# Kernel optimization log

Measured on AMD Instinct MI355X. Metric: run time of the kernel, lower is better.

The kernel has to match this reference:

```python
import jax, jax.numpy as jnp
import numpy as np

L, B, S, D, H, FF, V, P = 6, 8, 1024, 768, 12, 3072, 50257, 1024
DH = D // H
EPS = 1e-5


def setup_inputs() -> dict:
    key = jax.random.key(0)
    ks = jax.random.split(key, 12)
    std = 0.02
    return {
        "x_ids": jax.random.randint(ks[0], (B, S), 0, V),
        "calibrated_mask": jax.random.normal(ks[1], (B, S, S), jnp.float32),
        "wte": jax.random.normal(ks[2], (V, D), jnp.float32) * std,
        "wpe": jax.random.normal(ks[3], (P, D), jnp.float32) * std,
        "ln1_g": jnp.ones((L, D), jnp.float32),
        "ln1_b": jnp.zeros((L, D), jnp.float32),
        "qkv_w": jax.random.normal(ks[4], (L, D, 3 * D), jnp.float32) * std,
        "qkv_b": jnp.zeros((L, 3 * D), jnp.float32),
        "ao_w": jax.random.normal(ks[5], (L, D, D), jnp.float32) * std,
        "ao_b": jnp.zeros((L, D), jnp.float32),
        "ln2_g": jnp.ones((L, D), jnp.float32),
        "ln2_b": jnp.zeros((L, D), jnp.float32),
        "fc_w": jax.random.normal(ks[6], (L, D, FF), jnp.float32) * std,
        "fc_b": jnp.zeros((L, FF), jnp.float32),
        "op_w": jax.random.normal(ks[7], (L, FF, D), jnp.float32) * std,
        "op_b": jnp.zeros((L, D), jnp.float32),
        "lnf_g": jnp.ones((D,), jnp.float32),
        "lnf_b": jnp.zeros((D,), jnp.float32),
    }


def _ln(x, g, b):
    m = jnp.mean(x, axis=-1, keepdims=True)
    v = jnp.var(x, axis=-1, keepdims=True)
    return (x - m) * jax.lax.rsqrt(v + EPS) * g + b


def _gelu_new(x):
    c = np.sqrt(2.0 / np.pi).astype(np.float32)
    return 0.5 * x * (1.0 + jnp.tanh(c * (x + 0.044715 * x * x * x)))


def _gpt2_forward(x_ids, calibrated_mask, wte, wpe, ln1_g, ln1_b, qkv_w, qkv_b,
                  ao_w, ao_b, ln2_g, ln2_b, fc_w, fc_b, op_w, op_b, lnf_g, lnf_b):
    s = x_ids.shape[1]
    h = wte[x_ids] + wpe[:s][None, :, :]  # [B,S,D]
    causal = jnp.tril(jnp.ones((s, s), bool))
    neg = jnp.finfo(h.dtype).min
    # additive mask, broadcast over heads (unsqueeze(1).repeat over n_head)
    add_mask = calibrated_mask[:, None, :, :]  # [B,1,S,S]

    def block(hid, p):
        l1g, l1b, qw, qb, aw, ab, l2g, l2b, fw, fb, ow, ob = p
        x = _ln(hid, l1g, l1b)
        qkv = x @ qw + qb  # [B,S,3D]
        q, k, v = jnp.split(qkv, 3, axis=-1)
        q = q.reshape(q.shape[0], s, H, DH).transpose(0, 2, 1, 3)
        k = k.reshape(k.shape[0], s, H, DH).transpose(0, 2, 1, 3)
        v = v.reshape(v.shape[0], s, H, DH).transpose(0, 2, 1, 3)
        scores = jnp.einsum('bhqd,bhkd->bhqk', q, k) / jnp.sqrt(jnp.asarray(DH, q.dtype))
        scores = jnp.where(causal[None, None], scores, neg)
        scores = scores + add_mask
        w = jax.nn.softmax(scores, axis=-1)
        a = jnp.einsum('bhqk,bhkd->bhqd', w, v)
        a = a.transpose(0, 2, 1, 3).reshape(a.shape[0], s, D)
        hid = hid + a @ aw + ab
        x2 = _ln(hid, l2g, l2b)
        hid = hid + _gelu_new(x2 @ fw + fb) @ ow + ob
        return hid, None

    params = (ln1_g, ln1_b, qkv_w, qkv_b, ao_w, ao_b, ln2_g, ln2_b, fc_w, fc_b, op_w, op_b)
    h, _ = jax.lax.scan(block, h, params)
    return _ln(h, lnf_g, lnf_b)


def reference(x_ids, calibrated_mask, wte, wpe, ln1_g, ln1_b, qkv_w, qkv_b,
              ao_w, ao_b, ln2_g, ln2_b, fc_w, fc_b, op_w, op_b, lnf_g, lnf_b):
    return _gpt2_forward(x_ids, calibrated_mask, wte, wpe, ln1_g, ln1_b, qkv_w, qkv_b,
                         ao_w, ao_b, ln2_g, ln2_b, fc_w, fc_b, op_w, op_b, lnf_g, lnf_b)
```

## Files before the change

### kernel.cpp

```cpp
#include <hip/hip_runtime.h>
#include <hip/hip_bf16.h>

typedef __bf16 bf16_t;
typedef __bf16 bf16x8 __attribute__((ext_vector_type(8)));
typedef __bf16 bf16x4 __attribute__((ext_vector_type(4)));
typedef float  f32x4  __attribute__((ext_vector_type(4)));

#define DEV __device__ __forceinline__

DEV void gload_lds16(const void* g, void* l) {
  __builtin_amdgcn_global_load_lds(
      (__attribute__((address_space(1))) void*)(void*)g,
      (__attribute__((address_space(3))) void*)l, 16, 0, 0);
}

__global__ __launch_bounds__(256)
void transpose_cast(const float* __restrict__ in, bf16_t* __restrict__ out,
                    int K, int N) {
  __shared__ float tile[32][33];
  const long z = blockIdx.z;
  const float* inz = in + z * (long)K * N;
  bf16_t* outz = out + z * (long)N * K;
  const int k0 = blockIdx.x * 32;
  const int n0 = blockIdx.y * 32;
  const int tx = threadIdx.x;
  const int ty = threadIdx.y;
#pragma unroll
  for (int i = 0; i < 32; i += 8)
    tile[ty + i][tx] = inz[(long)(k0 + ty + i) * N + n0 + tx];
  __syncthreads();
#pragma unroll
  for (int i = 0; i < 32; i += 8)
    outz[(long)(n0 + ty + i) * K + k0 + tx] = (bf16_t)tile[tx][ty + i];
}

__global__ __launch_bounds__(256)
void embed_kernel(const int* __restrict__ ids, const float* __restrict__ wte,
                  const float* __restrict__ wpe, bf16_t* __restrict__ h) {
  const int t = blockIdx.x * 256 + threadIdx.x;
  const int row = t / 96;
  const int c8  = (t % 96) * 8;
  const int s   = row & 1023;
  const float* wr = wte + (long)ids[row] * 768 + c8;
  const float* pr = wpe + (long)s * 768 + c8;
  bf16x8 o;
#pragma unroll
  for (int j = 0; j < 8; ++j) o[j] = (bf16_t)(wr[j] + pr[j]);
  *(bf16x8*)&h[(long)row * 768 + c8] = o;
}

template <bool BF16OUT>
__global__ __launch_bounds__(256)
void ln_kernel(const bf16_t* __restrict__ x, const float* __restrict__ g,
               const float* __restrict__ b, bf16_t* __restrict__ ob,
               float* __restrict__ of) {
  const int lane = threadIdx.x & 63;
  const long row = blockIdx.x * 4 + (threadIdx.x >> 6);
  const bf16_t* xr = x + row * 768;
  const bf16x8 v8 = *(const bf16x8*)&xr[lane * 8];
  const bf16x4 v4 = *(const bf16x4*)&xr[512 + lane * 4];
  float vv[12];
#pragma unroll
  for (int j = 0; j < 8; ++j) vv[j] = (float)v8[j];
#pragma unroll
  for (int j = 0; j < 4; ++j) vv[8 + j] = (float)v4[j];
  float s = 0.f, sq = 0.f;
#pragma unroll
  for (int j = 0; j < 12; ++j) { s += vv[j]; sq += vv[j] * vv[j]; }
#pragma unroll
  for (int o = 32; o; o >>= 1) { s += __shfl_xor(s, o); sq += __shfl_xor(sq, o); }
  const float mean = s * (1.f / 768.f);
  const float rs = rsqrtf(sq * (1.f / 768.f) - mean * mean + 1e-5f);
  if (BF16OUT) {
    bf16x8 o8; bf16x4 o4;
#pragma unroll
    for (int j = 0; j < 8; ++j) {
      const int col = lane * 8 + j;
      o8[j] = (bf16_t)((vv[j] - mean) * rs * g[col] + b[col]);
    }
#pragma unroll
    for (int j = 0; j < 4; ++j) {
      const int col = 512 + lane * 4 + j;
      o4[j] = (bf16_t)((vv[8 + j] - mean) * rs * g[col] + b[col]);
    }
    *(bf16x8*)&ob[row * 768 + lane * 8] = o8;
    *(bf16x4*)&ob[row * 768 + 512 + lane * 4] = o4;
  } else {
#pragma unroll
    for (int j = 0; j < 8; ++j) {
      const int col = lane * 8 + j;
      of[row * 768 + col] = (vv[j] - mean) * rs * g[col] + b[col];
    }
#pragma unroll
    for (int j = 0; j < 4; ++j) {
      const int col = 512 + lane * 4 + j;
      of[row * 768 + col] = (vv[8 + j] - mean) * rs * g[col] + b[col];
    }
  }
}

template <int EPI, int BN>
__global__ __launch_bounds__(256, 4)
void gemm_bt(const bf16_t* __restrict__ A, const bf16_t* __restrict__ Bt,
             const float* __restrict__ bias, bf16_t* __restrict__ Cb,
             int M, int N, int K) {
  constexpr int NI = BN / 32;
  __shared__ bf16_t As[128 * 64];
  __shared__ bf16_t Bs[BN * 64];
  const int tid  = threadIdx.x;
  const int lane = tid & 63, w = tid >> 6;
  const int col = lane & 15, s16 = lane >> 4;
  const int nbn = N / BN;
  const int cpx = gridDim.x >> 3;
  const int bid = (blockIdx.x & 7) * cpx + (blockIdx.x >> 3);
  const int bm = bid / nbn, bn = bid % nbn;
  const int wr = w >> 1, wc = w & 1;

  f32x4 acc[4][NI];
#pragma unroll
  for (int i = 0; i < 4; ++i)
#pragma unroll
    for (int j = 0; j < NI; ++j) acc[i][j] = f32x4{0.f, 0.f, 0.f, 0.f};

  const long arow0 = (long)bm * 128;
  const long brow0 = (long)bn * BN;

  const int nt = K >> 6;
  for (int t = 0; t < nt; ++t) {
    const int k0 = t << 6;
#pragma unroll
    for (int i = 0; i < 4; ++i) {
      const int c = i * 256 + tid;
      const int row = c >> 3, slot = c & 7;
      gload_lds16(A + (arow0 + row) * (long)K + k0 + ((slot ^ (row & 7)) << 3),
                  (char*)As + c * 16);
    }
#pragma unroll
    for (int i = 0; i < BN / 32; ++i) {
      const int c = i * 256 + tid;
      const int row = c >> 3, slot = c & 7;
      gload_lds16(Bt + (brow0 + row) * (long)K + k0 + ((slot ^ (row & 7)) << 3),
                  (char*)Bs + c * 16);
    }
    __syncthreads();

    bf16x8 af[2][4], bfr[2][NI];
#pragma unroll
    for (int mi = 0; mi < 4; ++mi) {
      const int row = wr * 64 + mi * 16 + col;
#pragma unroll
      for (int ks = 0; ks < 2; ++ks) {
        const int slot = ks * 4 + s16;
        af[ks][mi] = *(const bf16x8*)((char*)As + row * 128 +
                                      ((slot ^ (row & 7)) << 4));
      }
    }
#pragma unroll
    for (int ni = 0; ni < NI; ++ni) {
      const int row = wc * (BN / 2) + ni * 16 + col;
#pragma unroll
      for (int ks = 0; ks < 2; ++ks) {
        const int slot = ks * 4 + s16;
        bfr[ks][ni] = *(const bf16x8*)((char*)Bs + row * 128 +
                                       ((slot ^ (row & 7)) << 4));
      }
    }
#pragma unroll
    for (int ks = 0; ks < 2; ++ks)
#pragma unroll
      for (int mi = 0; mi < 4; ++mi)
#pragma unroll
        for (int ni = 0; ni < NI; ++ni)
          acc[mi][ni] = __builtin_amdgcn_mfma_f32_16x16x32_bf16(
              af[ks][mi], bfr[ks][ni], acc[mi][ni], 0, 0, 0);

    __syncthreads();
  }

  const int colb = bn * BN + wc * (BN / 2) + col;
  const int rowb = bm * 128 + wr * 64 + (s16 << 2);
#pragma unroll
  for (int ni = 0; ni < NI; ++ni) {
    const int ccol = colb + ni * 16;
    const float bv = bias[ccol];
#pragma unroll
    for (int mi = 0; mi < 4; ++mi) {
      const int row = rowb + mi * 16;
#pragma unroll
      for (int r = 0; r < 4; ++r) {
        const float v = acc[mi][ni][r] + bv;
        const long idx = (long)(row + r) * N + ccol;
        if (EPI == 1) {
          Cb[idx] = (bf16_t)((float)Cb[idx] + v);
        } else if (EPI == 2) {
          Cb[idx] = (bf16_t)v;
        } else {
          const float z = 0.7978845608028654f * (v + 0.044715f * v * v * v);
          Cb[idx] = (bf16_t)(v / (1.f + __expf(-2.f * z)));
        }
      }
    }
  }
}

template <int EPI>
__global__ __launch_bounds__(512, 4)
void gemm_bw(const bf16_t* __restrict__ A, const bf16_t* __restrict__ Bt,
             const float* __restrict__ bias, bf16_t* __restrict__ Cb,
             int M, int N, int K) {
  __shared__ bf16_t As[256 * 64];
  __shared__ bf16_t Bs[128 * 64];
  const int tid = threadIdx.x;
  const int lane = tid & 63, w = tid >> 6;
  const int col = lane & 15, s16 = lane >> 4;
  const int wm = w >> 1, wn = w & 1;
  const int nbn = N >> 7;
  const int cpx = gridDim.x >> 3;
  const int bid = (blockIdx.x & 7) * cpx + (blockIdx.x >> 3);
  const int bm = bid / nbn, bn = bid % nbn;
  const long arow0 = (long)bm * 256, brow0 = (long)bn * 128;

  f32x4 acc[4][4];
#pragma unroll
  for (int i = 0; i < 4; ++i)
#pragma unroll
    for (int j = 0; j < 4; ++j) acc[i][j] = f32x4{0.f, 0.f, 0.f, 0.f};

  const int nt = K >> 6;
  for (int t = 0; t < nt; ++t) {
    const int k0 = t << 6;
#pragma unroll
    for (int i = 0; i < 4; ++i) {
      const int c = i * 512 + tid;
      const int row = c >> 3, slot = c & 7;
      gload_lds16(A + (arow0 + row) * (long)K + k0 + ((slot ^ (row & 7)) << 3),
                  (char*)As + c * 16);
    }
#pragma unroll
    for (int i = 0; i < 2; ++i) {
      const int c = i * 512 + tid;
      const int row = c >> 3, slot = c & 7;
      gload_lds16(Bt + (brow0 + row) * (long)K + k0 + ((slot ^ (row & 7)) << 3),
                  (char*)Bs + c * 16);
    }
    __syncthreads();

    bf16x8 af[2][4], bfr[2][4];
#pragma unroll
    for (int mi = 0; mi < 4; ++mi) {
      const int row = wm * 64 + mi * 16 + col;
#pragma unroll
      for (int ks = 0; ks < 2; ++ks) {
        const int slot = ks * 4 + s16;
        af[ks][mi] = *(const bf16x8*)((char*)As + row * 128 +
                                      ((slot ^ (row & 7)) << 4));
      }
    }
#pragma unroll
    for (int ni = 0; ni < 4; ++ni) {
      const int row = wn * 64 + ni * 16 + col;
#pragma unroll
      for (int ks = 0; ks < 2; ++ks) {
        const int slot = ks * 4 + s16;
        bfr[ks][ni] = *(const bf16x8*)((char*)Bs + row * 128 +
                                       ((slot ^ (row & 7)) << 4));
      }
    }
#pragma unroll
    for (int ks = 0; ks < 2; ++ks)
#pragma unroll
      for (int mi = 0; mi < 4; ++mi)
#pragma unroll
        for (int ni = 0; ni < 4; ++ni)
          acc[mi][ni] = __builtin_amdgcn_mfma_f32_16x16x32_bf16(
              af[ks][mi], bfr[ks][ni], acc[mi][ni], 0, 0, 0);

    __syncthreads();
  }

  const int rowb = bm * 256 + wm * 64 + (s16 << 2);
  const int colb = bn * 128 + wn * 64 + col;
#pragma unroll
  for (int ni = 0; ni < 4; ++ni) {
    const int ccol = colb + ni * 16;
    const float bv = bias[ccol];
#pragma unroll
    for (int mi = 0; mi < 4; ++mi) {
      const int row = rowb + mi * 16;
#pragma unroll
      for (int r = 0; r < 4; ++r) {
        const float v = acc[mi][ni][r] + bv;
        if (EPI == 2) Cb[(long)(row + r) * N + ccol] = (bf16_t)v;
        else {
          const float z = 0.7978845608028654f * (v + 0.044715f * v * v * v);
          Cb[(long)(row + r) * N + ccol] = (bf16_t)(v / (1.f + __expf(-2.f * z)));
        }
      }
    }
  }
}

__global__ __launch_bounds__(256, 3)
void attn_kernel(const bf16_t* __restrict__ qkv, const float* __restrict__ mask,
                 bf16_t* __restrict__ out) {
  __shared__ bf16_t Kl[2][64 * 64];
  __shared__ bf16_t Vt[2][64 * 64];
  __shared__ bf16_t Pl[4][16 * 64];
  const int tid = threadIdx.x, lane = tid & 63, w = tid >> 6;
  const int col = lane & 15, s16 = lane >> 4, l7 = lane & 7;
  const int qp = blockIdx.x & 7;
  const int bh = blockIdx.x >> 3;
  const int b = bh / 12, h = bh % 12;
  const int sw0 = (s16 ^ l7) << 4;
  const int sw1 = ((s16 + 4) ^ l7) << 4;
  char* const plw = (char*)&Pl[w][0];
  const long qkvb = (long)b * 1024 * 2304;

  auto stageK = [&](int buf, int k0) {
#pragma unroll
    for (int i = 0; i < 2; ++i) {
      const int c = i * 256 + tid;
      const int krow = c >> 3, slot = c & 7;
      gload_lds16(qkv + qkvb + (long)(k0 + krow) * 2304 + 768 + h * 64 +
                      ((slot ^ (krow & 7)) << 3),
                  (char*)&Kl[buf][0] + i * 4096 + w * 1024);
    }
  };
  auto loadV = [&](int k0, bf16x8& t0, bf16x8& t1) {
    const bf16_t* vbase = qkv + qkvb + 1536 + h * 64;
#pragma unroll
    for (int i = 0; i < 2; ++i) {
      const int c = i * 256 + tid;
      const int d = c & 63, koct = c >> 6;
      const bf16_t* vsrc = vbase + (long)(k0 + koct * 8) * 2304 + d;
      bf16x8 tv;
#pragma unroll
      for (int j = 0; j < 8; ++j) tv[j] = vsrc[(long)j * 2304];
      if (i == 0) t0 = tv; else t1 = tv;
    }
  };
  auto storeV = [&](int buf, const bf16x8& t0, const bf16x8& t1) {
#pragma unroll
    for (int i = 0; i < 2; ++i) {
      const int c = i * 256 + tid;
      const int d = c & 63, koct = c >> 6;
      *(bf16x8*)((char*)&Vt[buf][0] + d * 128 + ((koct ^ (d & 7)) << 4)) =
          (i == 0) ? t0 : t1;
    }
  };

#pragma unroll 1
  for (int pass = 0; pass < 2; ++pass) {
    const int qt = pass ? (15 - qp) : qp;
    const int qrow0 = qt * 64 + w * 16;
    const long rowQ = (long)(b * 1024 + qrow0 + col) * 2304 + h * 64;
    const bf16x8 aq0 = *(const bf16x8*)&qkv[rowQ + s16 * 8];
    const bf16x8 aq1 = *(const bf16x8*)&qkv[rowQ + 32 + s16 * 8];
    const int qb = qrow0 + s16 * 4;
    const float* mrow = mask + ((long)b * 1024 + qb) * 1024;

    auto loadM = [&](int k0, float (&m)[4][4]) {
#pragma unroll
      for (int g = 0; g < 4; ++g)
#pragma unroll
        for (int r = 0; r < 4; ++r)
          m[g][r] = mrow[(long)r * 1024 + k0 + g * 16 + col];
    };

    float m_run[4], l_run[4];
    f32x4 o_acc[4];
#pragma unroll
    for (int r = 0; r < 4; ++r) { m_run[r] = -INFINITY; l_run[r] = 0.f; }
#pragma unroll
    for (int go = 0; go < 4; ++go) o_acc[go] = f32x4{0.f, 0.f, 0.f, 0.f};

    bf16x8 tv0, tv1;
    stageK(0, 0);
    loadV(0, tv0, tv1);
    storeV(0, tv0, tv1);
    float msk[4][4];
    loadM(0, msk);
    __syncthreads();

#pragma unroll 1
    for (int kt = 0; kt <= qt; ++kt) {
      const int cur = kt & 1;
      const bool more = kt < qt;
      const int k0 = kt * 64;
      float mnx[4][4];
      if (more) {
        stageK(cur ^ 1, k0 + 64);
        loadV(k0 + 64, tv0, tv1);
        loadM(k0 + 64, mnx);
      }

      f32x4 sf[4];
      __builtin_amdgcn_s_setprio(1);
#pragma unroll
      for (int g = 0; g < 4; ++g) {
        const int rbyte = (g * 16 + col) * 128;
        bf16x8 bk0 = *(const bf16x8*)((char*)&Kl[cur][0] + rbyte + sw0);
        bf16x8 bk1 = *(const bf16x8*)((char*)&Kl[cur][0] + rbyte + sw1);
        f32x4 z = f32x4{0.f, 0.f, 0.f, 0.f};
        z = __builtin_amdgcn_mfma_f32_16x16x32_bf16(aq0, bk0, z, 0, 0, 0);
        z = __builtin_amdgcn_mfma_f32_16x16x32_bf16(aq1, bk1, z, 0, 0, 0);
        sf[g] = z;
      }
      __builtin_amdgcn_s_setprio(0);

      const bool diag = (kt == qt);
      float sv[4][4];
#pragma unroll
      for (int g = 0; g < 4; ++g)
#pragma unroll
        for (int r = 0; r < 4; ++r) {
          float s = sf[g][r] * 0.125f + msk[g][r];
          if (diag && (k0 + g * 16 + col) > (qb + r)) s = -INFINITY;
          sv[g][r] = s;
        }
#pragma unroll
      for (int r = 0; r < 4; ++r) {
        float mx = fmaxf(fmaxf(sv[0][r], sv[1][r]), fmaxf(sv[2][r], sv[3][r]));
#pragma unroll
        for (int o = 8; o; o >>= 1) mx = fmaxf(mx, __shfl_xor(mx, o));
        const float m_new = fmaxf(m_run[r], mx);
        const float f = __expf(m_run[r] - m_new);
        m_run[r] = m_new;
        float sum = 0.f;
#pragma unroll
        for (int g = 0; g < 4; ++g) {
          const float p = __expf(sv[g][r] - m_new);
          sv[g][r] = p;
          sum += p;
        }
#pragma unroll
        for (int o = 8; o; o >>= 1) sum += __shfl_xor(sum, o);
        l_run[r] = l_run[r] * f + sum;
#pragma unroll
        for (int go = 0; go < 4; ++go) o_acc[go][r] *= f;
      }

#pragma unroll
      for (int g = 0; g < 4; ++g) {
        const int ks = 2 * g + (col >> 3);
#pragma unroll
        for (int r = 0; r < 4; ++r) {
          const int qr = s16 * 4 + r;
          *(bf16_t*)(plw + qr * 128 + ((ks ^ (qr & 7)) << 4) + l7 * 2) = (bf16_t)sv[g][r];
        }
      }
      const bf16x8 pa0 = *(const bf16x8*)(plw + col * 128 + sw0);
      const bf16x8 pa1 = *(const bf16x8*)(plw + col * 128 + sw1);
      __builtin_amdgcn_s_setprio(1);
#pragma unroll
      for (int go = 0; go < 4; ++go) {
        const int dbyte = (go * 16 + col) * 128;
        bf16x8 bv0 = *(const bf16x8*)((char*)&Vt[cur][0] + dbyte + sw0);
        bf16x8 bv1 = *(const bf16x8*)((char*)&Vt[cur][0] + dbyte + sw1);
        o_acc[go] = __builtin_amdgcn_mfma_f32_16x16x32_bf16(pa0, bv0, o_acc[go], 0, 0, 0);
        o_acc[go] = __builtin_amdgcn_mfma_f32_16x16x32_bf16(pa1, bv1, o_acc[go], 0, 0, 0);
      }
      __builtin_amdgcn_s_setprio(0);

      if (more) {
        storeV(cur ^ 1, tv0, tv1);
#pragma unroll
        for (int g = 0; g < 4; ++g)
#pragma unroll
          for (int r = 0; r < 4; ++r) msk[g][r] = mnx[g][r];
      }
      __syncthreads();
    }

    float inv[4];
#pragma unroll
    for (int r = 0; r < 4; ++r) inv[r] = 1.f / l_run[r];
#pragma unroll
    for (int go = 0; go < 4; ++go)
#pragma unroll
      for (int r = 0; r < 4; ++r)
        out[(long)(b * 1024 + qb + r) * 768 + h * 64 + go * 16 + col] =
            (bf16_t)(o_acc[go][r] * inv[r]);
  }
}

extern "C" void kernel_launch(void* const* d_in, const int* in_sizes, int n_in,
                              void* d_out, int out_size, void* d_ws, size_t ws_size,
                              hipStream_t stream) {
  const int*   x_ids = (const int*)d_in[0];
  const float* mask  = (const float*)d_in[1];
  const float* wte   = (const float*)d_in[2];
  const float* wpe   = (const float*)d_in[3];
  const float* ln1_g = (const float*)d_in[4];
  const float* ln1_b = (const float*)d_in[5];
  const float* qkv_w = (const float*)d_in[6];
  const float* qkv_b = (const float*)d_in[7];
  const float* ao_w  = (const float*)d_in[8];
  const float* ao_b  = (const float*)d_in[9];
  const float* ln2_g = (const float*)d_in[10];
  const float* ln2_b = (const float*)d_in[11];
  const float* fc_w  = (const float*)d_in[12];
  const float* fc_b  = (const float*)d_in[13];
  const float* op_w  = (const float*)d_in[14];
  const float* op_b  = (const float*)d_in[15];
  const float* lnf_g = (const float*)d_in[16];
  const float* lnf_b = (const float*)d_in[17];

  char* ws = (char*)d_ws;
  size_t off = 0;
  auto alloc = [&](size_t bytes) {
    char* p = ws + off;
    off += (bytes + 255) & ~(size_t)255;
    return p;
  };
  bf16_t* wqT = (bf16_t*)alloc(6ull * 2304 * 768 * 2);
  bf16_t* waT = (bf16_t*)alloc(6ull * 768 * 768 * 2);
  bf16_t* wfT = (bf16_t*)alloc(6ull * 3072 * 768 * 2);
  bf16_t* woT = (bf16_t*)alloc(6ull * 768 * 3072 * 2);
  bf16_t* h   = (bf16_t*)alloc(8192ull * 768 * 2);
  bf16_t* xb  = (bf16_t*)alloc(8192ull * 768 * 2);
  bf16_t* qkv = (bf16_t*)alloc(8192ull * 2304 * 2);
  bf16_t* abf = (bf16_t*)alloc(8192ull * 768 * 2);
  bf16_t* fb  = (bf16_t*)alloc(8192ull * 3072 * 2);
  if (off > ws_size) return;

  const dim3 tb(32, 8);
  transpose_cast<<<dim3(768 / 32, 2304 / 32, 6), tb, 0, stream>>>(qkv_w, wqT, 768, 2304);
  transpose_cast<<<dim3(768 / 32, 768 / 32, 6), tb, 0, stream>>>(ao_w, waT, 768, 768);
  transpose_cast<<<dim3(768 / 32, 3072 / 32, 6), tb, 0, stream>>>(fc_w, wfT, 768, 3072);
  transpose_cast<<<dim3(3072 / 32, 768 / 32, 6), tb, 0, stream>>>(op_w, woT, 3072, 768);

  embed_kernel<<<3072, 256, 0, stream>>>(x_ids, wte, wpe, h);

  for (int l = 0; l < 6; ++l) {
    ln_kernel<true><<<2048, 256, 0, stream>>>(h, ln1_g + l * 768, ln1_b + l * 768, xb, nullptr);
    gemm_bw<2><<<576, 512, 0, stream>>>(xb, wqT + (long)l * 2304 * 768,
                                        qkv_b + l * 2304, qkv, 8192, 2304, 768);
    attn_kernel<<<768, 256, 0, stream>>>(qkv, mask, abf);
    gemm_bt<1, 64><<<768, 256, 0, stream>>>(abf, waT + (long)l * 768 * 768,
                                            ao_b + l * 768, h, 8192, 768, 768);
    ln_kernel<true><<<2048, 256, 0, stream>>>(h, ln2_g + l * 768, ln2_b + l * 768, xb, nullptr);
    gemm_bw<3><<<768, 512, 0, stream>>>(xb, wfT + (long)l * 3072 * 768,
                                        fc_b + l * 3072, fb, 8192, 3072, 768);
    gemm_bt<1, 64><<<768, 256, 0, stream>>>(fb, woT + (long)l * 768 * 3072,
                                            op_b + l * 768, h, 8192, 768, 3072);
  }

  ln_kernel<false><<<2048, 256, 0, stream>>>(h, lnf_g, lnf_b, nullptr, (float*)d_out);
}
```

Baseline: 1.600 ms.

## Double-buffer LDS tiles in both GEMM kernels to overlap loads with MFMA

Both bf16 GEMM kernels now keep two LDS buffers for the A and B tiles. The next K-tile's async global_load_lds is issued before the current tile is computed, and a manual vmcnt wait plus a raw s_barrier replaces __syncthreads. The aim is to hide global-memory latency behind MFMA work. In exchange, LDS use per block doubles, which can cut the number of resident blocks per CU. The hardcoded vmcnt(6) assumes a specific number of loads per stage, so it only waits correctly for some tile widths.

```diff
diff --git a/kernel.cpp b/kernel.cpp
--- a/kernel.cpp
+++ b/kernel.cpp
@@ -13,6 +13,9 @@
       (__attribute__((address_space(1))) void*)(void*)g,
       (__attribute__((address_space(3))) void*)l, 16, 0, 0);
 }
+
+#define FENCE() asm volatile("" ::: "memory")
+#define BARRIER() do { FENCE(); __builtin_amdgcn_s_barrier(); FENCE(); } while (0)
 
 __global__ __launch_bounds__(256)
 void transpose_cast(const float* __restrict__ in, bf16_t* __restrict__ out,
@@ -105,8 +108,8 @@
              const float* __restrict__ bias, bf16_t* __restrict__ Cb,
              int M, int N, int K) {
   constexpr int NI = BN / 32;
-  __shared__ bf16_t As[128 * 64];
-  __shared__ bf16_t Bs[BN * 64];
+  __shared__ bf16_t As[2][128 * 64];
+  __shared__ bf16_t Bs[2][BN * 64];
   const int tid  = threadIdx.x;
   const int lane = tid & 63, w = tid >> 6;
   const int col = lane & 15, s16 = lane >> 4;
@@ -125,24 +128,35 @@
   const long arow0 = (long)bm * 128;
   const long brow0 = (long)bn * BN;
 
-  const int nt = K >> 6;
-  for (int t = 0; t < nt; ++t) {
-    const int k0 = t << 6;
+  auto stage = [&](int buf, int k0) {
 #pragma unroll
     for (int i = 0; i < 4; ++i) {
       const int c = i * 256 + tid;
       const int row = c >> 3, slot = c & 7;
       gload_lds16(A + (arow0 + row) * (long)K + k0 + ((slot ^ (row & 7)) << 3),
-                  (char*)As + c * 16);
+                  (char*)&As[buf][0] + c * 16);
     }
 #pragma unroll
     for (int i = 0; i < BN / 32; ++i) {
       const int c = i * 256 + tid;
       const int row = c >> 3, slot = c & 7;
       gload_lds16(Bt + (brow0 + row) * (long)K + k0 + ((slot ^ (row & 7)) << 3),
-                  (char*)Bs + c * 16);
-    }
-    __syncthreads();
+                  (char*)&Bs[buf][0] + c * 16);
+    }
+  };
+
+  const int nt = K >> 6;
+  stage(0, 0);
+  int cur = 0;
+  for (int t = 0; t < nt; ++t) {
+    if (t + 1 < nt) {
+      stage(cur ^ 1, (t + 1) << 6);
+      asm volatile("s_waitcnt vmcnt(6)" ::: "memory");
+    } else {
+      asm volatile("s_waitcnt vmcnt(0)" ::: "memory");
+    }
+    __builtin_amdgcn_sched_barrier(0);
+    BARRIER();
 
     bf16x8 af[2][4], bfr[2][NI];
 #pragma unroll
@@ -151,7 +165,7 @@
 #pragma unroll
       for (int ks = 0; ks < 2; ++ks) {
         const int slot = ks * 4 + s16;
-        af[ks][mi] = *(const bf16x8*)((char*)As + row * 128 +
+        af[ks][mi] = *(const bf16x8*)((char*)&As[cur][0] + row * 128 +
                                       ((slot ^ (row & 7)) << 4));
       }
     }
@@ -161,7 +175,7 @@
 #pragma unroll
       for (int ks = 0; ks < 2; ++ks) {
         const int slot = ks * 4 + s16;
-        bfr[ks][ni] = *(const bf16x8*)((char*)Bs + row * 128 +
+        bfr[ks][ni] = *(const bf16x8*)((char*)&Bs[cur][0] + row * 128 +
                                        ((slot ^ (row & 7)) << 4));
       }
     }
@@ -174,7 +188,8 @@
           acc[mi][ni] = __builtin_amdgcn_mfma_f32_16x16x32_bf16(
               af[ks][mi], bfr[ks][ni], acc[mi][ni], 0, 0, 0);
 
-    __syncthreads();
+    BARRIER();
+    cur ^= 1;
   }
 
   const int colb = bn * BN + wc * (BN / 2) + col;
@@ -208,8 +223,8 @@
 void gemm_bw(const bf16_t* __restrict__ A, const bf16_t* __restrict__ Bt,
              const float* __restrict__ bias, bf16_t* __restrict__ Cb,
              int M, int N, int K) {
-  __shared__ bf16_t As[256 * 64];
-  __shared__ bf16_t Bs[128 * 64];
+  __shared__ bf16_t As[2][256 * 64];
+  __shared__ bf16_t Bs[2][128 * 64];
   const int tid = threadIdx.x;
   const int lane = tid & 63, w = tid >> 6;
   const int col = lane & 15, s16 = lane >> 4;
@@ -226,24 +241,35 @@
 #pragma unroll
     for (int j = 0; j < 4; ++j) acc[i][j] = f32x4{0.f, 0.f, 0.f, 0.f};
 
-  const int nt = K >> 6;
-  for (int t = 0; t < nt; ++t) {
-    const int k0 = t << 6;
+  auto stage = [&](int buf, int k0) {
 #pragma unroll
     for (int i = 0; i < 4; ++i) {
       const int c = i * 512 + tid;
       const int row = c >> 3, slot = c & 7;
       gload_lds16(A + (arow0 + row) * (long)K + k0 + ((slot ^ (row & 7)) << 3),
-                  (char*)As + c * 16);
+                  (char*)&As[buf][0] + c * 16);
     }
 #pragma unroll
     for (int i = 0; i < 2; ++i) {
       const int c = i * 512 + tid;
       const int row = c >> 3, slot = c & 7;
       gload_lds16(Bt + (brow0 + row) * (long)K + k0 + ((slot ^ (row & 7)) << 3),
-                  (char*)Bs + c * 16);
-    }
-    __syncthreads();
+                  (char*)&Bs[buf][0] + c * 16);
+    }
+  };
+
+  const int nt = K >> 6;
+  stage(0, 0);
+  int cur = 0;
+  for (int t = 0; t < nt; ++t) {
+    if (t + 1 < nt) {
+      stage(cur ^ 1, (t + 1) << 6);
+      asm volatile("s_waitcnt vmcnt(6)" ::: "memory");
+    } else {
+      asm volatile("s_waitcnt vmcnt(0)" ::: "memory");
+    }
+    __builtin_amdgcn_sched_barrier(0);
+    BARRIER();
 
     bf16x8 af[2][4], bfr[2][4];
 #pragma unroll
@@ -252,7 +278,7 @@
 #pragma unroll
       for (int ks = 0; ks < 2; ++ks) {
         const int slot = ks * 4 + s16;
-        af[ks][mi] = *(const bf16x8*)((char*)As + row * 128 +
+        af[ks][mi] = *(const bf16x8*)((char*)&As[cur][0] + row * 128 +
                                       ((slot ^ (row & 7)) << 4));
       }
     }
@@ -262,7 +288,7 @@
 #pragma unroll
       for (int ks = 0; ks < 2; ++ks) {
         const int slot = ks * 4 + s16;
-        bfr[ks][ni] = *(const bf16x8*)((char*)Bs + row * 128 +
+        bfr[ks][ni] = *(const bf16x8*)((char*)&Bs[cur][0] + row * 128 +
                                        ((slot ^ (row & 7)) << 4));
       }
     }
@@ -275,7 +301,8 @@
           acc[mi][ni] = __builtin_amdgcn_mfma_f32_16x16x32_bf16(
               af[ks][mi], bfr[ks][ni], acc[mi][ni], 0, 0, 0);
 
-    __syncthreads();
+    BARRIER();
+    cur ^= 1;
   }
 
   const int rowb = bm * 256 + wm * 64 + (s16 << 2);
```

New measurement: 1.723 ms. 1.08x slower.

## Load A fragments directly from global in gemm_bt and vectorize weight transpose

Applied to the files above, without the earlier changes.

The narrow-N GEMM no longer stages the A tile in LDS. Each wave loads its A fragments straight from global memory into registers, and only B goes through LDS. This cuts LDS traffic and footprint, at the cost of less coalesced global loads of A and no prefetch overlap. The weight transpose kernel is also changed to use 4-wide float loads and 4-wide bf16 stores with a 1D thread block.

```diff
diff --git a/kernel.cpp b/kernel.cpp
--- a/kernel.cpp
+++ b/kernel.cpp
@@ -23,15 +23,16 @@
   bf16_t* outz = out + z * (long)N * K;
   const int k0 = blockIdx.x * 32;
   const int n0 = blockIdx.y * 32;
-  const int tx = threadIdx.x;
-  const int ty = threadIdx.y;
-#pragma unroll
-  for (int i = 0; i < 32; i += 8)
-    tile[ty + i][tx] = inz[(long)(k0 + ty + i) * N + n0 + tx];
+  const int tx = threadIdx.x & 7;
+  const int ty = threadIdx.x >> 3;
+  const f32x4 ld = *(const f32x4*)&inz[(long)(k0 + ty) * N + n0 + tx * 4];
+#pragma unroll
+  for (int j = 0; j < 4; ++j) tile[ty][tx * 4 + j] = ld[j];
   __syncthreads();
-#pragma unroll
-  for (int i = 0; i < 32; i += 8)
-    outz[(long)(n0 + ty + i) * K + k0 + tx] = (bf16_t)tile[tx][ty + i];
+  bf16x4 st;
+#pragma unroll
+  for (int j = 0; j < 4; ++j) st[j] = (bf16_t)tile[tx * 4 + j][ty];
+  *(bf16x4*)&outz[(long)(n0 + ty) * K + k0 + tx * 4] = st;
 }
 
 __global__ __launch_bounds__(256)
@@ -99,44 +100,43 @@
   }
 }
 
-template <int EPI, int BN>
+template <int EPI>
 __global__ __launch_bounds__(256, 4)
 void gemm_bt(const bf16_t* __restrict__ A, const bf16_t* __restrict__ Bt,
              const float* __restrict__ bias, bf16_t* __restrict__ Cb,
              int M, int N, int K) {
-  constexpr int NI = BN / 32;
-  __shared__ bf16_t As[128 * 64];
-  __shared__ bf16_t Bs[BN * 64];
+  __shared__ bf16_t Bs[64 * 64];
   const int tid  = threadIdx.x;
   const int lane = tid & 63, w = tid >> 6;
   const int col = lane & 15, s16 = lane >> 4;
-  const int nbn = N / BN;
+  const int nbn = N >> 6;
   const int cpx = gridDim.x >> 3;
   const int bid = (blockIdx.x & 7) * cpx + (blockIdx.x >> 3);
   const int bm = bid / nbn, bn = bid % nbn;
   const int wr = w >> 1, wc = w & 1;
 
-  f32x4 acc[4][NI];
+  f32x4 acc[4][2];
 #pragma unroll
   for (int i = 0; i < 4; ++i)
 #pragma unroll
-    for (int j = 0; j < NI; ++j) acc[i][j] = f32x4{0.f, 0.f, 0.f, 0.f};
+    for (int j = 0; j < 2; ++j) acc[i][j] = f32x4{0.f, 0.f, 0.f, 0.f};
 
   const long arow0 = (long)bm * 128;
-  const long brow0 = (long)bn * BN;
+  const long brow0 = (long)bn * 64;
+  const bf16_t* aBase = A + (arow0 + wr * 64 + col) * (long)K;
 
   const int nt = K >> 6;
   for (int t = 0; t < nt; ++t) {
     const int k0 = t << 6;
-#pragma unroll
-    for (int i = 0; i < 4; ++i) {
-      const int c = i * 256 + tid;
-      const int row = c >> 3, slot = c & 7;
-      gload_lds16(A + (arow0 + row) * (long)K + k0 + ((slot ^ (row & 7)) << 3),
-                  (char*)As + c * 16);
-    }
-#pragma unroll
-    for (int i = 0; i < BN / 32; ++i) {
+    bf16x8 af[2][4];
+#pragma unroll
+    for (int mi = 0; mi < 4; ++mi)
+#pragma unroll
+      for (int ks = 0; ks < 2; ++ks)
+        af[ks][mi] = *(const bf16x8*)&aBase[(long)(mi * 16) * K + k0 +
+                                            (ks * 4 + s16) * 8];
+#pragma unroll
+    for (int i = 0; i < 2; ++i) {
       const int c = i * 256 + tid;
       const int row = c >> 3, slot = c & 7;
       gload_lds16(Bt + (brow0 + row) * (long)K + k0 + ((slot ^ (row & 7)) << 3),
@@ -144,20 +144,10 @@
     }
     __syncthreads();
 
-    bf16x8 af[2][4], bfr[2][NI];
-#pragma unroll
-    for (int mi = 0; mi < 4; ++mi) {
-      const int row = wr * 64 + mi * 16 + col;
-#pragma unroll
-      for (int ks = 0; ks < 2; ++ks) {
-        const int slot = ks * 4 + s16;
-        af[ks][mi] = *(const bf16x8*)((char*)As + row * 128 +
-                                      ((slot ^ (row & 7)) << 4));
-      }
-    }
-#pragma unroll
-    for (int ni = 0; ni < NI; ++ni) {
-      const int row = wc * (BN / 2) + ni * 16 + col;
+    bf16x8 bfr[2][2];
+#pragma unroll
+    for (int ni = 0; ni < 2; ++ni) {
+      const int row = wc * 32 + ni * 16 + col;
 #pragma unroll
       for (int ks = 0; ks < 2; ++ks) {
         const int slot = ks * 4 + s16;
@@ -170,17 +160,17 @@
 #pragma unroll
       for (int mi = 0; mi < 4; ++mi)
 #pragma unroll
-        for (int ni = 0; ni < NI; ++ni)
+        for (int ni = 0; ni < 2; ++ni)
           acc[mi][ni] = __builtin_amdgcn_mfma_f32_16x16x32_bf16(
               af[ks][mi], bfr[ks][ni], acc[mi][ni], 0, 0, 0);
 
     __syncthreads();
   }
 
-  const int colb = bn * BN + wc * (BN / 2) + col;
+  const int colb = bn * 64 + wc * 32 + col;
   const int rowb = bm * 128 + wr * 64 + (s16 << 2);
 #pragma unroll
-  for (int ni = 0; ni < NI; ++ni) {
+  for (int ni = 0; ni < 2; ++ni) {
     const int ccol = colb + ni * 16;
     const float bv = bias[ccol];
 #pragma unroll
@@ -524,11 +514,10 @@
   bf16_t* fb  = (bf16_t*)alloc(8192ull * 3072 * 2);
   if (off > ws_size) return;
 
-  const dim3 tb(32, 8);
-  transpose_cast<<<dim3(768 / 32, 2304 / 32, 6), tb, 0, stream>>>(qkv_w, wqT, 768, 2304);
-  transpose_cast<<<dim3(768 / 32, 768 / 32, 6), tb, 0, stream>>>(ao_w, waT, 768, 768);
-  transpose_cast<<<dim3(768 / 32, 3072 / 32, 6), tb, 0, stream>>>(fc_w, wfT, 768, 3072);
-  transpose_cast<<<dim3(3072 / 32, 768 / 32, 6), tb, 0, stream>>>(op_w, woT, 3072, 768);
+  transpose_cast<<<dim3(768 / 32, 2304 / 32, 6), 256, 0, stream>>>(qkv_w, wqT, 768, 2304);
+  transpose_cast<<<dim3(768 / 32, 768 / 32, 6), 256, 0, stream>>>(ao_w, waT, 768, 768);
+  transpose_cast<<<dim3(768 / 32, 3072 / 32, 6), 256, 0, stream>>>(fc_w, wfT, 768, 3072);
+  transpose_cast<<<dim3(3072 / 32, 768 / 32, 6), 256, 0, stream>>>(op_w, woT, 3072, 768);
 
   embed_kernel<<<3072, 256, 0, stream>>>(x_ids, wte, wpe, h);
 
@@ -537,13 +526,13 @@
     gemm_bw<2><<<576, 512, 0, stream>>>(xb, wqT + (long)l * 2304 * 768,
                                         qkv_b + l * 2304, qkv, 8192, 2304, 768);
     attn_kernel<<<768, 256, 0, stream>>>(qkv, mask, abf);
-    gemm_bt<1, 64><<<768, 256, 0, stream>>>(abf, waT + (long)l * 768 * 768,
-                                            ao_b + l * 768, h, 8192, 768, 768);
+    gemm_bt<1><<<768, 256, 0, stream>>>(abf, waT + (long)l * 768 * 768,
+                                        ao_b + l * 768, h, 8192, 768, 768);
     ln_kernel<true><<<2048, 256, 0, stream>>>(h, ln2_g + l * 768, ln2_b + l * 768, xb, nullptr);
     gemm_bw<3><<<768, 512, 0, stream>>>(xb, wfT + (long)l * 3072 * 768,
                                         fc_b + l * 3072, fb, 8192, 3072, 768);
-    gemm_bt<1, 64><<<768, 256, 0, stream>>>(fb, woT + (long)l * 768 * 3072,
-                                            op_b + l * 768, h, 8192, 768, 3072);
+    gemm_bt<1><<<768, 256, 0, stream>>>(fb, woT + (long)l * 768 * 3072,
+                                        op_b + l * 768, h, 8192, 768, 3072);
   }
 
   ln_kernel<false><<<2048, 256, 0, stream>>>(h, lnf_g, lnf_b, nullptr, (float*)d_out);
```

Result: slower. 2.311 ms (+44.5%).
